# Performance work log

Measured on AMD Instinct MI355X. Metric: run time of the kernel, lower is better.

## Reference

```python
import jax, jax.numpy as jnp
import numpy as np

EPS_BN = 1e-4


def gcn_conv(x, W, b, src, dst):
    """PyG GCNConv with added self-loops and symmetric normalization."""
    N = x.shape[0]
    h = x @ W  # [N, out]
    # degree over targets, +1 for the implicit self-loop on every node
    deg = jnp.zeros((N,), x.dtype).at[dst].add(1.0) + 1.0
    dinv = jax.lax.rsqrt(deg)  # deg^{-1/2}
    norm = dinv[src] * dinv[dst]  # per-edge coefficient
    msg = h[src] * norm[:, None]  # [E, out] gather (memory-bound)
    out = jax.ops.segment_sum(msg, dst, num_segments=N)
    out = out + h * (dinv * dinv)[:, None]  # self-loop term, norm = 1/deg
    return out + b


def batch_norm(x, gamma, beta):
    # training-mode BN over the node dim, biased variance (matches torch train)
    m = jnp.mean(x, axis=0)
    v = jnp.mean(jnp.square(x - m), axis=0)
    return (x - m) * jax.lax.rsqrt(v + EPS_BN) * gamma + beta


def setup_inputs() -> dict:
    key = jax.random.key(0)
    ks = jax.random.split(key, 8)
    N, E, D = 100000, 1600000, 64
    L = 2
    x = jax.random.normal(ks[0], (N, D), jnp.float32)
    edge_index = jax.random.randint(ks[1], (2, E), 0, N, jnp.int32)
    batch = jnp.sort(jax.random.randint(ks[2], (N,), 0, 128, jnp.int32))
    s = 1.0 / np.sqrt(D)
    return {
        "x": x,
        "edge_index": edge_index,
        "batch": batch,
        "enc_W": jax.random.normal(ks[3], (L, D, D), jnp.float32) * s,
        "enc_b": jnp.zeros((L, D), jnp.float32),
        "enc_gamma": jnp.ones((L, D), jnp.float32),
        "enc_beta": jnp.zeros((L, D), jnp.float32),
        "attr_W": jax.random.normal(ks[4], (L, D, D), jnp.float32) * s,
        "attr_b": jnp.zeros((L, D), jnp.float32),
        "attr_gamma": jnp.ones((L, D), jnp.float32),
        "attr_beta": jnp.zeros((L, D), jnp.float32),
        "str_W": jax.random.normal(ks[5], (L, D, D), jnp.float32) * s,
        "str_b": jnp.zeros((L, D), jnp.float32),
        "str_gamma": jnp.ones((L, D), jnp.float32),
        "str_beta": jnp.zeros((L, D), jnp.float32),
    }


def reference(x, edge_index, batch, enc_W, enc_b, enc_gamma, enc_beta,
              attr_W, attr_b, attr_gamma, attr_beta,
              str_W, str_b, str_gamma, str_beta):
    src, dst = edge_index[0], edge_index[1]
    L = enc_W.shape[0]

    # ---- Encoder: GCN -> sigmoid -> (dropout id) -> BN ----
    h = x
    for i in range(L):
        h = gcn_conv(h, enc_W[i], enc_b[i], src, dst)
        h = jax.nn.sigmoid(h)
        h = batch_norm(h, enc_gamma[i], enc_beta[i])
    x_enc = h
    # x_pool = global_mean_pool(x_enc, batch) is computed but discarded upstream

    # ---- Attribute decoder: GCN -> (dropout) -> sigmoid (except last) -> BN ----
    h = x_enc
    for i in range(L):
        h = gcn_conv(h, attr_W[i], attr_b[i], src, dst)
        if i != L - 1:
            h = jax.nn.sigmoid(h)
        h = batch_norm(h, attr_gamma[i], attr_beta[i])
    x_att = h

    # ---- Structure decoder ----
    h = x_enc
    for i in range(L):
        h = gcn_conv(h, str_W[i], str_b[i], src, dst)
        if i != L - 1:
            h = jax.nn.sigmoid(h)
        else:
            h = jax.nn.sigmoid(h * 0.5)
        h = batch_norm(h, str_gamma[i], str_beta[i])
    x_str = h

    return (x_str, x_att, x_enc)
```

## Files before the change

### kernel.cpp

```cpp
#include <hip/hip_runtime.h>

#define D 64
#define BCH 4096

typedef __attribute__((ext_vector_type(8))) _Float16 f16x8;
typedef __attribute__((ext_vector_type(4))) float f32x4;

__device__ __forceinline__ float sigmoidf_(float x) {
    return 1.0f / (1.0f + __expf(-x));
}
__device__ __forceinline__ float h2f(ushort u) {
    _Float16 h;
    __builtin_memcpy(&h, &u, 2);
    return (float)h;
}
__device__ __forceinline__ ushort f2h(float f) {
    _Float16 h = (_Float16)f;
    ushort u;
    __builtin_memcpy(&u, &h, 2);
    return u;
}
__device__ __forceinline__ float2 up2(uint v) {
    float2 r;
    r.x = h2f((ushort)(v & 0xffffu));
    r.y = h2f((ushort)(v >> 16));
    return r;
}


__global__ __launch_bounds__(256) void bin_edges(const int* __restrict__ src,
                                                 const int* __restrict__ dst,
                                                 int* __restrict__ bcur,
                                                 int* __restrict__ binsrc,
                                                 int* __restrict__ bindst,
                                                 int CAP, int E) {
    __shared__ int lsrc[BCH], ldst[BCH];
    __shared__ int hist[128], base[128];
    int t = threadIdx.x;
    int e0 = blockIdx.x * BCH;
    if (t < 128) hist[t] = 0;
    __syncthreads();
    for (int k = t; k < BCH; k += 256) {
        int e = e0 + k;
        int d_ = -1, s_ = 0;
        if (e < E) {
            s_ = src[e];
            d_ = dst[e];
            atomicAdd(&hist[d_ >> 10], 1);
        }
        lsrc[k] = s_;
        ldst[k] = d_;
    }
    __syncthreads();
    if (t < 128) {
        int c = hist[t];
        base[t] = (c > 0) ? atomicAdd(&bcur[t], c) : 0;
        hist[t] = 0;
    }
    __syncthreads();
    for (int k = t; k < BCH; k += 256) {
        int d_ = ldst[k];
        if (d_ >= 0) {
            int b = d_ >> 10;
            int p = base[b] + atomicAdd(&hist[b], 1);
            binsrc[(size_t)b * CAP + p] = lsrc[k];
            bindst[(size_t)b * CAP + p] = d_;
        }
    }
}

__global__ __launch_bounds__(128) void scan_nb(const int* __restrict__ bcur,
                                               int* __restrict__ boff,
                                               int* __restrict__ csr,
                                               int NB, int N, int E) {
    __shared__ int tmp[128];
    int t = threadIdx.x;
    int v = (t < NB) ? bcur[t] : 0;
    tmp[t] = v;
    __syncthreads();
    for (int o = 1; o < 128; o <<= 1) {
        int x = (t >= o) ? tmp[t - o] : 0;
        __syncthreads();
        tmp[t] += x;
        __syncthreads();
    }
    if (t < NB) boff[t] = tmp[t] - v;
    if (t == 0) csr[N] = E;
}

__global__ __launch_bounds__(256) void build_csr(const int* __restrict__ binsrc,
                                                 const int* __restrict__ bindst,
                                                 const int* __restrict__ bcur,
                                                 const int* __restrict__ boff,
                                                 int* __restrict__ csr,
                                                 int* __restrict__ sorted,
                                                 float* __restrict__ dinv,
                                                 float* __restrict__ rdinv,
                                                 int CAP, int N) {
    __shared__ int hist[1024];
    __shared__ int part[256];
    int t = threadIdx.x;
    int b = blockIdx.x;
    int nb0 = b << 10;
    int cnt = bcur[b];
    int e0 = boff[b];
    const int* bs = binsrc + (size_t)b * CAP;
    const int* bd = bindst + (size_t)b * CAP;
    for (int k = t; k < 1024; k += 256) hist[k] = 0;
    __syncthreads();
    for (int k = t; k < cnt; k += 256) atomicAdd(&hist[bd[k] - nb0], 1);
    __syncthreads();
    int v0 = hist[4 * t], v1 = hist[4 * t + 1], v2 = hist[4 * t + 2], v3 = hist[4 * t + 3];
    part[t] = v0 + v1 + v2 + v3;
    __syncthreads();
    for (int o = 1; o < 256; o <<= 1) {
        int x = (t >= o) ? part[t - o] : 0;
        __syncthreads();
        part[t] += x;
        __syncthreads();
    }
    int run = (t > 0) ? part[t - 1] : 0;
    int pre[4];
    pre[0] = run;
    pre[1] = run + v0;
    pre[2] = run + v0 + v1;
    pre[3] = run + v0 + v1 + v2;
    int deg[4] = {v0, v1, v2, v3};
    __syncthreads();
    hist[4 * t + 0] = e0 + pre[0];
    hist[4 * t + 1] = e0 + pre[1];
    hist[4 * t + 2] = e0 + pre[2];
    hist[4 * t + 3] = e0 + pre[3];
#pragma unroll
    for (int j = 0; j < 4; j++) {
        int node = nb0 + 4 * t + j;
        if (node < N) {
            csr[node] = e0 + pre[j];
            float c = (float)deg[j] + 1.0f;
            dinv[node] = rsqrtf(c);
            rdinv[node] = sqrtf(c);
        }
    }
    __syncthreads();
    for (int k = t; k < cnt; k += 256) {
        int d_ = bd[k];
        int p = atomicAdd(&hist[d_ - nb0], 1);
        sorted[p] = bs[k];
    }
}


__global__ __launch_bounds__(256) void prep_xd(const float* __restrict__ x,
                                               const float* __restrict__ dinv,
                                               ushort* __restrict__ actd, int N16) {
    int p = blockIdx.x * 256 + threadIdx.x;
    if (p >= N16) return;
    int n = p >> 4;
    float d = dinv[n];
    float4 v = reinterpret_cast<const float4*>(x)[p];
    ushort4 o;
    o.x = f2h(v.x * d);
    o.y = f2h(v.y * d);
    o.z = f2h(v.z * d);
    o.w = f2h(v.w * d);
    reinterpret_cast<ushort4*>(actd)[p] = o;
}

__global__ __launch_bounds__(256) void wprep(const float* __restrict__ W,
                                             const float* __restrict__ Aaf,
                                             ushort* __restrict__ wfrag) {
    int idx = blockIdx.x * 256 + threadIdx.x;
    if (idx >= 4096) return;
    int i = idx & 7;
    int lane = (idx >> 3) & 63;
    int hc = idx >> 9;
    int h = hc >> 2, c = hc & 3;
    int k = h * 32 + (lane >> 4) * 8 + i;
    int j = c * 16 + (lane & 15);
    float w = W[k * 64 + j];
    if (Aaf) w *= Aaf[k];
    wfrag[idx] = f2h(w);
}


__global__ __launch_bounds__(256) void agg_g(const ushort* __restrict__ actd,
                                             const int* __restrict__ ptr,
                                             const int* __restrict__ srcs,
                                             const float* __restrict__ dinv,
                                             const float* __restrict__ rdinv,
                                             ushort* __restrict__ zh,
                                             float* __restrict__ ssum,
                                             float* __restrict__ sssq,
                                             float* __restrict__ qout, int N) {
    __shared__ float red[2][4][64];
    int lane = threadIdx.x & 63;
    int wv = threadIdx.x >> 6;
    int l = lane & 31, h = lane >> 5;
    const bool do_stats = (ssum != nullptr);
    const bool do_q = (qout != nullptr);
    float2 ps = make_float2(0.f, 0.f), pq = make_float2(0.f, 0.f);
    for (int n = blockIdx.x * 4 + wv; n < N; n += gridDim.x * 4) {
        int s = ptr[n], e = ptr[n + 1];
        uint selfu = *reinterpret_cast<const uint*>(actd + ((size_t)n << 6) + (l << 1));
        float2 sf = up2(selfu);
        float2 acc = (h == 0) ? sf : make_float2(0.f, 0.f);
        float dn = dinv[n];
        if (do_stats && h == 0) {
            float r = rdinv[n];
            float ax = sf.x * r, ay = sf.y * r;
            ps.x += ax; ps.y += ay;
            pq.x += ax * ax; pq.y += ay * ay;
        }
        float qa = 0.f;
        int i = s + h;
        for (; i + 6 < e; i += 8) {
            int u0 = srcs[i], u1 = srcs[i + 2], u2 = srcs[i + 4], u3 = srcs[i + 6];
            uint w0 = *reinterpret_cast<const uint*>(actd + ((size_t)u0 << 6) + (l << 1));
            uint w1 = *reinterpret_cast<const uint*>(actd + ((size_t)u1 << 6) + (l << 1));
            uint w2 = *reinterpret_cast<const uint*>(actd + ((size_t)u2 << 6) + (l << 1));
            uint w3 = *reinterpret_cast<const uint*>(actd + ((size_t)u3 << 6) + (l << 1));
            if (do_q && l == 0) qa += (dinv[u0] + dinv[u1]) + (dinv[u2] + dinv[u3]);
            float2 f0 = up2(w0), f1 = up2(w1), f2 = up2(w2), f3 = up2(w3);
            acc.x += (f0.x + f1.x) + (f2.x + f3.x);
            acc.y += (f0.y + f1.y) + (f2.y + f3.y);
        }
        for (; i < e; i += 2) {
            int u = srcs[i];
            uint w = *reinterpret_cast<const uint*>(actd + ((size_t)u << 6) + (l << 1));
            if (do_q && l == 0) qa += dinv[u];
            float2 f = up2(w);
            acc.x += f.x;
            acc.y += f.y;
        }
        acc.x += __shfl_xor(acc.x, 32);
        acc.y += __shfl_xor(acc.y, 32);
        if (do_q) {
            float qo = qa + __shfl(qa, 32);
            if (lane == 0) qout[n] = dn * (dn + qo);
        }
        if (h == 0) {
            uint pk = (uint)f2h(acc.x * dn) | ((uint)f2h(acc.y * dn) << 16);
            *reinterpret_cast<uint*>(zh + ((size_t)n << 6) + (l << 1)) = pk;
        }
    }
    if (do_stats) {
        if (h == 0) {
            red[0][wv][2 * l + 0] = ps.x;
            red[0][wv][2 * l + 1] = ps.y;
            red[1][wv][2 * l + 0] = pq.x;
            red[1][wv][2 * l + 1] = pq.y;
        }
        __syncthreads();
        if (wv == 0) {
            float t0 = red[0][0][lane] + red[0][1][lane] + red[0][2][lane] + red[0][3][lane];
            float t1 = red[1][0][lane] + red[1][1][lane] + red[1][2][lane] + red[1][3][lane];
            atomicAdd(&ssum[lane], t0);
            atomicAdd(&sssq[lane], t1);
        }
    }
}

__global__ __launch_bounds__(256) void agg_dual(const ushort* __restrict__ ab,
                                                const int* __restrict__ ptr,
                                                const int* __restrict__ srcs,
                                                const float* __restrict__ dinv,
                                                const float* __restrict__ rdinv,
                                                ushort* __restrict__ zab,
                                                float* __restrict__ ssA,
                                                float* __restrict__ sqA,
                                                float* __restrict__ ssS,
                                                float* __restrict__ sqS,
                                                int N, int E) {
    __shared__ float red[2][4][128];
    int lane = threadIdx.x & 63;
    int wv = threadIdx.x >> 6;
    int Em1 = E - 1;
    float2 ps = make_float2(0.f, 0.f), pq = make_float2(0.f, 0.f);
    for (int n = blockIdx.x * 4 + wv; n < N; n += gridDim.x * 4) {
        int s = ptr[n], e = ptr[n + 1];
        uint su = *reinterpret_cast<const uint*>(ab + ((size_t)n << 7) + (lane << 1));
        float2 acc = up2(su);
        {
            float r = rdinv[n];
            float ax = acc.x * r, ay = acc.y * r;
            ps.x += ax; ps.y += ay;
            pq.x += ax * ax; pq.y += ay * ay;
        }
        int i = s;
        for (; i + 7 < e; i += 8) {
            int u[8];
#pragma unroll
            for (int j = 0; j < 8; j++) u[j] = srcs[i + j];
#pragma unroll
            for (int j = 0; j < 8; j++) {
                uint v = *reinterpret_cast<const uint*>(ab + ((size_t)u[j] << 7) + (lane << 1));
                float2 f = up2(v);
                acc.x += f.x;
                acc.y += f.y;
            }
        }
        if (i < e) {
#pragma unroll
            for (int j = 0; j < 8; j++) {
                int idx = min(i + j, Em1);
                int u_ = srcs[idx];
                uint v = *reinterpret_cast<const uint*>(ab + ((size_t)u_ << 7) + (lane << 1));
                float w = (i + j < e) ? 1.0f : 0.0f;
                float2 f = up2(v);
                acc.x = fmaf(w, f.x, acc.x);
                acc.y = fmaf(w, f.y, acc.y);
            }
        }
        float dn = dinv[n];
        uint pk = (uint)f2h(acc.x * dn) | ((uint)f2h(acc.y * dn) << 16);
        *reinterpret_cast<uint*>(zab + ((size_t)n << 7) + (lane << 1)) = pk;
    }
    red[0][wv][2 * lane + 0] = ps.x;
    red[0][wv][2 * lane + 1] = ps.y;
    red[1][wv][2 * lane + 0] = pq.x;
    red[1][wv][2 * lane + 1] = pq.y;
    __syncthreads();
    if (wv == 0) {
#pragma unroll
        for (int m0 = 0; m0 < 2; m0++) {
            int m = lane + m0 * 64;
            float t0 = red[0][0][m] + red[0][1][m] + red[0][2][m] + red[0][3][m];
            float t1 = red[1][0][m] + red[1][1][m] + red[1][2][m] + red[1][3][m];
            if (m < 64) {
                atomicAdd(&ssA[m], t0);
                atomicAdd(&sqA[m], t1);
            } else {
                atomicAdd(&ssS[m - 64], t0);
                atomicAdd(&sqS[m - 64], t1);
            }
        }
    }
}


template <int MODE, bool HAS_AFF, bool OUT_HALF>
__global__ __launch_bounds__(256) void gemm_mfma(const ushort* __restrict__ zh, int is,
                                                 const ushort* __restrict__ wfrag,
                                                 const float* __restrict__ bias,
                                                 const float* __restrict__ u,
                                                 const float* __restrict__ q,
                                                 const float* __restrict__ dinv,
                                                 ushort* __restrict__ outh, int os,
                                                 float* __restrict__ outf,
                                                 float* __restrict__ ssum,
                                                 float* __restrict__ sssq, int N) {
    int tid = threadIdx.x;
    int lane = tid & 63;
    int wv = tid >> 6;
    int l15 = lane & 15;
    int lg = lane >> 4;
    int tb = blockIdx.x * 64;

    const ushort* zrow = zh + (size_t)(tb + wv * 16 + l15) * is + (lg << 3);
    f16x8 a0 = *reinterpret_cast<const f16x8*>(zrow);
    f16x8 a1 = *reinterpret_cast<const f16x8*>(zrow + 32);

    const f16x8* wf = reinterpret_cast<const f16x8*>(wfrag) + lane;

    f32x4 acc[4];
#pragma unroll
    for (int c = 0; c < 4; c++) {
        f32x4 t = {0.f, 0.f, 0.f, 0.f};
        t = __builtin_amdgcn_mfma_f32_16x16x32_f16(a0, wf[(0 * 4 + c) * 64], t, 0, 0, 0);
        t = __builtin_amdgcn_mfma_f32_16x16x32_f16(a1, wf[(1 * 4 + c) * 64], t, 0, 0, 0);
        acc[c] = t;
    }

    int rowbase = tb + wv * 16 + lg * 4;
    float qv[4], dv[4];
    bool vld[4];
#pragma unroll
    for (int r = 0; r < 4; r++) {
        int row = rowbase + r;
        vld[r] = row < N;
        qv[r] = (HAS_AFF && vld[r]) ? q[row] : 0.f;
        dv[r] = (OUT_HALF && vld[r]) ? dinv[row] : 0.f;
    }
    float sa[4], sq[4];
#pragma unroll
    for (int c = 0; c < 4; c++) { sa[c] = 0.f; sq[c] = 0.f; }

#pragma unroll
    for (int c = 0; c < 4; c++) {
        int col = c * 16 + l15;
        float bcol = bias[col];
        float ucol = HAS_AFF ? u[col] : 0.f;
#pragma unroll
        for (int r = 0; r < 4; r++) {
            if (!vld[r]) continue;
            float o = acc[c][r] + bcol;
            if (HAS_AFF) o = fmaf(qv[r], ucol, o);
            float a = (MODE == 0) ? sigmoidf_(o)
                                  : ((MODE == 1) ? o : sigmoidf_(0.5f * o));
            int row = rowbase + r;
            if (OUT_HALF) {
                outh[(size_t)row * os + col] = f2h(a * dv[r]);
            } else {
                outf[((size_t)row << 6) + col] = a;
                sa[c] += a;
                sq[c] += a * a;
            }
        }
    }

    if (!OUT_HALF) {
        __shared__ float red[2][4][4][16];
#pragma unroll
        for (int c = 0; c < 4; c++) {
            sa[c] += __shfl_xor(sa[c], 16);
            sa[c] += __shfl_xor(sa[c], 32);
            sq[c] += __shfl_xor(sq[c], 16);
            sq[c] += __shfl_xor(sq[c], 32);
        }
        if (lg == 0) {
#pragma unroll
            for (int c = 0; c < 4; c++) {
                red[0][wv][c][l15] = sa[c];
                red[1][wv][c][l15] = sq[c];
            }
        }
        __syncthreads();
        if (wv == 0) {
            int c = lane >> 4, l = lane & 15;
            float t0 = red[0][0][c][l] + red[0][1][c][l] + red[0][2][c][l] + red[0][3][c][l];
            float t1 = red[1][0][c][l] + red[1][1][c][l] + red[1][2][c][l] + red[1][3][c][l];
            atomicAdd(&ssum[lane], t0);
            atomicAdd(&sssq[lane], t1);
        }
    }
}


__global__ __launch_bounds__(64) void finalize_aff(const float* __restrict__ ssum,
                                                   const float* __restrict__ sssq,
                                                   const float* __restrict__ gamma,
                                                   const float* __restrict__ beta,
                                                   float* __restrict__ A,
                                                   float* __restrict__ C, float invN) {
    int c = threadIdx.x;
    float m = ssum[c] * invN;
    float var = sssq[c] * invN - m * m;
    float rs = rsqrtf(var + 1e-4f);
    float a = rs * gamma[c];
    A[c] = a;
    C[c] = fmaf(-m, a, beta[c]);
}

__global__ __launch_bounds__(64) void compute_u(const float* __restrict__ C,
                                                const float* __restrict__ W,
                                                float* __restrict__ u) {
    int j = threadIdx.x;
    float s = 0.f;
    for (int k = 0; k < 64; k++) s = fmaf(C[k], W[k * 64 + j], s);
    u[j] = s;
}

__global__ __launch_bounds__(256) void bn_apply_h(const ushort* __restrict__ actd,
                                                  const float* __restrict__ rdinv,
                                                  const float* __restrict__ A,
                                                  const float* __restrict__ C,
                                                  float* __restrict__ out, int N16) {
    int p = blockIdx.x * 256 + threadIdx.x;
    if (p >= N16) return;
    int n = p >> 4;
    int cb = (p & 15) * 4;
    float r = rdinv[n];
    ushort4 v = reinterpret_cast<const ushort4*>(actd)[p];
    float4 o;
    o.x = fmaf(h2f(v.x) * r, A[cb + 0], C[cb + 0]);
    o.y = fmaf(h2f(v.y) * r, A[cb + 1], C[cb + 1]);
    o.z = fmaf(h2f(v.z) * r, A[cb + 2], C[cb + 2]);
    o.w = fmaf(h2f(v.w) * r, A[cb + 3], C[cb + 3]);
    reinterpret_cast<float4*>(out)[p] = o;
}

__global__ __launch_bounds__(256) void bn_apply_f32(const float* __restrict__ act,
                                                    const float* __restrict__ A,
                                                    const float* __restrict__ C,
                                                    float* __restrict__ out, int N16) {
    int p = blockIdx.x * 256 + threadIdx.x;
    if (p >= N16) return;
    int cb = (p & 15) * 4;
    float4 v = reinterpret_cast<const float4*>(act)[p];
    float4 o;
    o.x = fmaf(v.x, A[cb + 0], C[cb + 0]);
    o.y = fmaf(v.y, A[cb + 1], C[cb + 1]);
    o.z = fmaf(v.z, A[cb + 2], C[cb + 2]);
    o.w = fmaf(v.w, A[cb + 3], C[cb + 3]);
    reinterpret_cast<float4*>(out)[p] = o;
}


extern "C" void kernel_launch(void* const* d_in, const int* in_sizes, int n_in,
                              void* d_out, int out_size, void* d_ws, size_t ws_size,
                              hipStream_t stream) {
    const int N = in_sizes[0] / D;
    const int E = in_sizes[1] / 2;

    const float* x = (const float*)d_in[0];
    const int* ei = (const int*)d_in[1];
    const int* src_in = ei;
    const int* dst_in = ei + E;
    const float* encW = (const float*)d_in[3];
    const float* encb = (const float*)d_in[4];
    const float* encg = (const float*)d_in[5];
    const float* encbe = (const float*)d_in[6];
    const float* attW = (const float*)d_in[7];
    const float* attb = (const float*)d_in[8];
    const float* attg = (const float*)d_in[9];
    const float* attbe = (const float*)d_in[10];
    const float* strW = (const float*)d_in[11];
    const float* strb = (const float*)d_in[12];
    const float* strg = (const float*)d_in[13];
    const float* strbe = (const float*)d_in[14];

    const int NB = (N + 1023) >> 10;
    int CAP = (E + NB - 1) / NB;
    CAP = CAP + CAP / 8 + 256;
    CAP = (CAP + 255) & ~255;

    char* ws = (char*)d_ws;
    size_t off = 0;
    auto alloc = [&](size_t bytes) -> char* {
        char* p = ws + off;
        off += (bytes + 255) & ~(size_t)255;
        return p;
    };
    int* csr = (int*)alloc((size_t)(N + 1) * 4);
    int* bcur = (int*)alloc(128 * 4);
    int* boff = (int*)alloc(128 * 4);
    float* dinv = (float*)alloc((size_t)N * 4);
    float* rdinv = (float*)alloc((size_t)N * 4);
    float* q = (float*)alloc((size_t)N * 4);
    float* stats = (float*)alloc(6 * 128 * 4);
    float* aff = (float*)alloc(6 * 128 * 4);
    float* ubuf = (float*)alloc(6 * 64 * 4);
    ushort* wf = (ushort*)alloc(6 * 4096 * 2);
    int* sorted = (int*)alloc((size_t)E * 4);
    ushort* zh = (ushort*)alloc((size_t)(N + 64) * 64 * 2);
    size_t binbytes = 2 * (size_t)NB * CAP * 4;
    size_t zabbytes = (size_t)(N + 64) * 128 * 2;
    char* region = alloc(binbytes > zabbytes ? binbytes : zabbytes);
    int* binsrc = (int*)region;
    int* bindst = binsrc + (size_t)NB * CAP;
    ushort* zab = (ushort*)region;
    float* fbuf = (float*)alloc((size_t)N * 64 * 4);
    ushort* hB = (ushort*)fbuf;
    ushort* hA = hB + (size_t)N * 64;
    ushort* hAB = (ushort*)alloc((size_t)(N + 64) * 128 * 2);

    float* out_str = (float*)d_out;
    float* out_att = out_str + (size_t)N * D;
    float* out_enc = out_att + (size_t)N * D;

    hipMemsetAsync(bcur, 0, 128 * 4, stream);
    hipMemsetAsync(stats, 0, 6 * 128 * 4, stream);

    int N16 = N * 16;
    int g16 = (N16 + 255) / 256;
    int gT = (N + 63) / 64;
    float invN = 1.0f / (float)N;

    float* A0 = aff + 0 * 128; float* C0 = A0 + 64;
    float* A1 = aff + 1 * 128; float* C1 = A1 + 64;
    float* A2 = aff + 2 * 128; float* C2 = A2 + 64;
    float* A3 = aff + 3 * 128; float* C3 = A3 + 64;
    float* A4 = aff + 4 * 128; float* C4 = A4 + 64;
    float* A5 = aff + 5 * 128; float* C5 = A5 + 64;
    ushort* wf0 = wf + 0 * 4096;
    ushort* wf1 = wf + 1 * 4096;
    ushort* wf2 = wf + 2 * 4096;
    ushort* wf3 = wf + 3 * 4096;
    ushort* wf4 = wf + 4 * 4096;
    ushort* wf5 = wf + 5 * 4096;

    bin_edges<<<(E + BCH - 1) / BCH, 256, 0, stream>>>(src_in, dst_in, bcur,
                                                       binsrc, bindst, CAP, E);
    scan_nb<<<1, 128, 0, stream>>>(bcur, boff, csr, NB, N, E);
    build_csr<<<NB, 256, 0, stream>>>(binsrc, bindst, bcur, boff, csr, sorted,
                                      dinv, rdinv, CAP, N);

    prep_xd<<<g16, 256, 0, stream>>>(x, dinv, hA, N16);
    wprep<<<16, 256, 0, stream>>>(encW, nullptr, wf0);
    agg_g<<<2048, 256, 0, stream>>>(hA, csr, sorted, dinv, rdinv, zh,
                                    nullptr, nullptr, q, N);
    gemm_mfma<0, false, true><<<gT, 256, 0, stream>>>(zh, 64, wf0, encb, nullptr,
                                                      q, dinv, hB, 64, nullptr,
                                                      nullptr, nullptr, N);
    agg_g<<<2048, 256, 0, stream>>>(hB, csr, sorted, dinv, rdinv, zh,
                                    stats + 0, stats + 64, nullptr, N);
    finalize_aff<<<1, 64, 0, stream>>>(stats + 0, stats + 64, encg, encbe, A0, C0, invN);
    compute_u<<<1, 64, 0, stream>>>(C0, encW + 4096, ubuf + 0);
    wprep<<<16, 256, 0, stream>>>(encW + 4096, A0, wf1);
    gemm_mfma<0, true, true><<<gT, 256, 0, stream>>>(zh, 64, wf1, encb + 64, ubuf + 0,
                                                     q, dinv, hA, 64, nullptr,
                                                     nullptr, nullptr, N);
    agg_g<<<2048, 256, 0, stream>>>(hA, csr, sorted, dinv, rdinv, zh,
                                    stats + 128, stats + 192, nullptr, N);
    finalize_aff<<<1, 64, 0, stream>>>(stats + 128, stats + 192, encg + 64,
                                       encbe + 64, A1, C1, invN);
    compute_u<<<1, 64, 0, stream>>>(C1, attW, ubuf + 64);
    compute_u<<<1, 64, 0, stream>>>(C1, strW, ubuf + 128);
    wprep<<<16, 256, 0, stream>>>(attW, A1, wf2);
    wprep<<<16, 256, 0, stream>>>(strW, A1, wf3);
    bn_apply_h<<<g16, 256, 0, stream>>>(hA, rdinv, A1, C1, out_enc, N16);
    gemm_mfma<0, true, true><<<gT, 256, 0, stream>>>(zh, 64, wf2, attb, ubuf + 64,
                                                     q, dinv, hAB, 128, nullptr,
                                                     nullptr, nullptr, N);
    gemm_mfma<0, true, true><<<gT, 256, 0, stream>>>(zh, 64, wf3, strb, ubuf + 128,
                                                     q, dinv, hAB + 64, 128, nullptr,
                                                     nullptr, nullptr, N);
    agg_dual<<<2048, 256, 0, stream>>>(hAB, csr, sorted, dinv, rdinv, zab,
                                       stats + 256, stats + 320,
                                       stats + 512, stats + 576, N, E);
    finalize_aff<<<1, 64, 0, stream>>>(stats + 256, stats + 320, attg, attbe,
                                       A2, C2, invN);
    compute_u<<<1, 64, 0, stream>>>(C2, attW + 4096, ubuf + 192);
    wprep<<<16, 256, 0, stream>>>(attW + 4096, A2, wf4);
    gemm_mfma<1, true, false><<<gT, 256, 0, stream>>>(zab, 128, wf4, attb + 64,
                                                      ubuf + 192, q, dinv,
                                                      nullptr, 0, fbuf,
                                                      stats + 384, stats + 448, N);
    finalize_aff<<<1, 64, 0, stream>>>(stats + 384, stats + 448, attg + 64,
                                       attbe + 64, A3, C3, invN);
    bn_apply_f32<<<g16, 256, 0, stream>>>(fbuf, A3, C3, out_att, N16);
    finalize_aff<<<1, 64, 0, stream>>>(stats + 512, stats + 576, strg, strbe,
                                       A4, C4, invN);
    compute_u<<<1, 64, 0, stream>>>(C4, strW + 4096, ubuf + 320);
    wprep<<<16, 256, 0, stream>>>(strW + 4096, A4, wf5);
    gemm_mfma<2, true, false><<<gT, 256, 0, stream>>>(zab + 64, 128, wf5, strb + 64,
                                                      ubuf + 320, q, dinv,
                                                      nullptr, 0, fbuf,
                                                      stats + 640, stats + 704, N);
    finalize_aff<<<1, 64, 0, stream>>>(stats + 640, stats + 704, strg + 64,
                                       strbe + 64, A5, C5, invN);
    bn_apply_f32<<<g16, 256, 0, stream>>>(fbuf, A5, C5, out_str, N16);
}
```

Before: 651.4 us.

## Fuse BN prep kernels, merge decoder GEMMs, recompute final GEMMs instead of f32 roundtrip

Merges finalize_aff, compute_u and wprep into a single layer_prep kernel per layer, cutting small-kernel launches. The two first-layer decoder GEMMs become one gemm_dual kernel that reads zh once. The final GEMMs now run twice: once to gather BN statistics and once to write the normalized output directly, replacing the f32 intermediate buffer and the bn_apply_f32 pass. agg_g and agg_dual load source indices eight at a time with readlane and prefetch the next batch, and agg_g switches to one 16-bit element per lane across all 64 lanes instead of two-halves-per-edge processing.

```diff
diff --git a/kernel.cpp b/kernel.cpp
--- a/kernel.cpp
+++ b/kernel.cpp
@@ -167,7 +167,6 @@
 }
 
 __global__ __launch_bounds__(256) void wprep(const float* __restrict__ W,
-                                             const float* __restrict__ Aaf,
                                              ushort* __restrict__ wfrag) {
     int idx = blockIdx.x * 256 + threadIdx.x;
     if (idx >= 4096) return;
@@ -177,9 +176,62 @@
     int h = hc >> 2, c = hc & 3;
     int k = h * 32 + (lane >> 4) * 8 + i;
     int j = c * 16 + (lane & 15);
-    float w = W[k * 64 + j];
-    if (Aaf) w *= Aaf[k];
-    wfrag[idx] = f2h(w);
+    wfrag[idx] = f2h(W[k * 64 + j]);
+}
+
+__global__ __launch_bounds__(256) void layer_prep(const float* __restrict__ ssum,
+                                                  const float* __restrict__ sssq,
+                                                  const float* __restrict__ gamma,
+                                                  const float* __restrict__ beta,
+                                                  const float* __restrict__ W,
+                                                  float* __restrict__ A,
+                                                  float* __restrict__ C,
+                                                  float* __restrict__ u,
+                                                  ushort* __restrict__ wfrag,
+                                                  float invN) {
+    __shared__ float As[64], Cs[64];
+    int t = threadIdx.x;
+    if (t < 64) {
+        float m = ssum[t] * invN;
+        float var = sssq[t] * invN - m * m;
+        float rs = rsqrtf(var + 1e-4f);
+        float a = rs * gamma[t];
+        As[t] = a;
+        A[t] = a;
+        float c = fmaf(-m, a, beta[t]);
+        Cs[t] = c;
+        C[t] = c;
+    }
+    __syncthreads();
+    if (t < 64) {
+        float s = 0.f;
+        for (int k = 0; k < 64; k++) s = fmaf(Cs[k], W[k * 64 + t], s);
+        u[t] = s;
+    }
+    for (int idx = t; idx < 4096; idx += 256) {
+        int i = idx & 7;
+        int lane = (idx >> 3) & 63;
+        int hc = idx >> 9;
+        int h = hc >> 2, c = hc & 3;
+        int k = h * 32 + (lane >> 4) * 8 + i;
+        int j = c * 16 + (lane & 15);
+        wfrag[idx] = f2h(W[k * 64 + j] * As[k]);
+    }
+}
+
+__global__ __launch_bounds__(64) void finalize_aff(const float* __restrict__ ssum,
+                                                   const float* __restrict__ sssq,
+                                                   const float* __restrict__ gamma,
+                                                   const float* __restrict__ beta,
+                                                   float* __restrict__ A,
+                                                   float* __restrict__ C, float invN) {
+    int c = threadIdx.x;
+    float m = ssum[c] * invN;
+    float var = sssq[c] * invN - m * m;
+    float rs = rsqrtf(var + 1e-4f);
+    float a = rs * gamma[c];
+    A[c] = a;
+    C[c] = fmaf(-m, a, beta[c]);
 }
 
 
@@ -191,65 +243,56 @@
                                              ushort* __restrict__ zh,
                                              float* __restrict__ ssum,
                                              float* __restrict__ sssq,
-                                             float* __restrict__ qout, int N) {
+                                             float* __restrict__ qout, int N, int E) {
     __shared__ float red[2][4][64];
     int lane = threadIdx.x & 63;
     int wv = threadIdx.x >> 6;
-    int l = lane & 31, h = lane >> 5;
+    int Em1 = E - 1;
     const bool do_stats = (ssum != nullptr);
     const bool do_q = (qout != nullptr);
-    float2 ps = make_float2(0.f, 0.f), pq = make_float2(0.f, 0.f);
+    float ps = 0.f, pq = 0.f;
     for (int n = blockIdx.x * 4 + wv; n < N; n += gridDim.x * 4) {
         int s = ptr[n], e = ptr[n + 1];
-        uint selfu = *reinterpret_cast<const uint*>(actd + ((size_t)n << 6) + (l << 1));
-        float2 sf = up2(selfu);
-        float2 acc = (h == 0) ? sf : make_float2(0.f, 0.f);
+        float self = h2f(actd[((size_t)n << 6) + lane]);
+        float acc = self;
         float dn = dinv[n];
-        if (do_stats && h == 0) {
-            float r = rdinv[n];
-            float ax = sf.x * r, ay = sf.y * r;
-            ps.x += ax; ps.y += ay;
-            pq.x += ax * ax; pq.y += ay * ay;
+        if (do_stats) {
+            float a = self * rdinv[n];
+            ps += a;
+            pq += a * a;
         }
         float qa = 0.f;
-        int i = s + h;
-        for (; i + 6 < e; i += 8) {
-            int u0 = srcs[i], u1 = srcs[i + 2], u2 = srcs[i + 4], u3 = srcs[i + 6];
-            uint w0 = *reinterpret_cast<const uint*>(actd + ((size_t)u0 << 6) + (l << 1));
-            uint w1 = *reinterpret_cast<const uint*>(actd + ((size_t)u1 << 6) + (l << 1));
-            uint w2 = *reinterpret_cast<const uint*>(actd + ((size_t)u2 << 6) + (l << 1));
-            uint w3 = *reinterpret_cast<const uint*>(actd + ((size_t)u3 << 6) + (l << 1));
-            if (do_q && l == 0) qa += (dinv[u0] + dinv[u1]) + (dinv[u2] + dinv[u3]);
-            float2 f0 = up2(w0), f1 = up2(w1), f2 = up2(w2), f3 = up2(w3);
-            acc.x += (f0.x + f1.x) + (f2.x + f3.x);
-            acc.y += (f0.y + f1.y) + (f2.y + f3.y);
-        }
-        for (; i < e; i += 2) {
-            int u = srcs[i];
-            uint w = *reinterpret_cast<const uint*>(actd + ((size_t)u << 6) + (l << 1));
-            if (do_q && l == 0) qa += dinv[u];
-            float2 f = up2(w);
-            acc.x += f.x;
-            acc.y += f.y;
-        }
-        acc.x += __shfl_xor(acc.x, 32);
-        acc.y += __shfl_xor(acc.y, 32);
-        if (do_q) {
-            float qo = qa + __shfl(qa, 32);
-            if (lane == 0) qout[n] = dn * (dn + qo);
-        }
-        if (h == 0) {
-            uint pk = (uint)f2h(acc.x * dn) | ((uint)f2h(acc.y * dn) << 16);
-            *reinterpret_cast<uint*>(zh + ((size_t)n << 6) + (l << 1)) = pk;
-        }
+        int i = s;
+        int idx8 = srcs[min(i + (lane & 7), Em1)];
+        while (i + 8 <= e) {
+            int ni = i + 8;
+            int nidx = srcs[min(ni + (lane & 7), Em1)];
+#pragma unroll
+            for (int j = 0; j < 8; j++) {
+                int u = __builtin_amdgcn_readlane(idx8, j);
+                float f = h2f(actd[((size_t)u << 6) + lane]);
+                acc += f;
+                if (do_q) qa += dinv[u];
+            }
+            idx8 = nidx;
+            i = ni;
+        }
+        if (i < e) {
+#pragma unroll
+            for (int j = 0; j < 8; j++) {
+                int u = __builtin_amdgcn_readlane(idx8, j);
+                float f = h2f(actd[((size_t)u << 6) + lane]);
+                float w = (i + j < e) ? 1.0f : 0.0f;
+                acc = fmaf(w, f, acc);
+                if (do_q) qa = fmaf(w, dinv[u], qa);
+            }
+        }
+        if (do_q && lane == 0) qout[n] = dn * (dn + qa);
+        zh[((size_t)n << 6) + lane] = f2h(acc * dn);
     }
     if (do_stats) {
-        if (h == 0) {
-            red[0][wv][2 * l + 0] = ps.x;
-            red[0][wv][2 * l + 1] = ps.y;
-            red[1][wv][2 * l + 0] = pq.x;
-            red[1][wv][2 * l + 1] = pq.y;
-        }
+        red[0][wv][lane] = ps;
+        red[1][wv][lane] = pq;
         __syncthreads();
         if (wv == 0) {
             float t0 = red[0][0][lane] + red[0][1][lane] + red[0][2][lane] + red[0][3][lane];
@@ -287,24 +330,26 @@
             pq.x += ax * ax; pq.y += ay * ay;
         }
         int i = s;
-        for (; i + 7 < e; i += 8) {
-            int u[8];
-#pragma unroll
-            for (int j = 0; j < 8; j++) u[j] = srcs[i + j];
+        int idx8 = srcs[min(i + (lane & 7), Em1)];
+        while (i + 8 <= e) {
+            int ni = i + 8;
+            int nidx = srcs[min(ni + (lane & 7), Em1)];
 #pragma unroll
             for (int j = 0; j < 8; j++) {
-                uint v = *reinterpret_cast<const uint*>(ab + ((size_t)u[j] << 7) + (lane << 1));
+                int u = __builtin_amdgcn_readlane(idx8, j);
+                uint v = *reinterpret_cast<const uint*>(ab + ((size_t)u << 7) + (lane << 1));
                 float2 f = up2(v);
                 acc.x += f.x;
                 acc.y += f.y;
             }
+            idx8 = nidx;
+            i = ni;
         }
         if (i < e) {
 #pragma unroll
             for (int j = 0; j < 8; j++) {
-                int idx = min(i + j, Em1);
-                int u_ = srcs[idx];
-                uint v = *reinterpret_cast<const uint*>(ab + ((size_t)u_ << 7) + (lane << 1));
+                int u = __builtin_amdgcn_readlane(idx8, j);
+                uint v = *reinterpret_cast<const uint*>(ab + ((size_t)u << 7) + (lane << 1));
                 float w = (i + j < e) ? 1.0f : 0.0f;
                 float2 f = up2(v);
                 acc.x = fmaf(w, f.x, acc.x);
@@ -337,8 +382,7 @@
     }
 }
 
-
-template <int MODE, bool HAS_AFF, bool OUT_HALF>
+template <int MODE, bool HAS_AFF, int OM>
 __global__ __launch_bounds__(256) void gemm_mfma(const ushort* __restrict__ zh, int is,
                                                  const ushort* __restrict__ wfrag,
                                                  const float* __restrict__ bias,
@@ -347,8 +391,8 @@
                                                  const float* __restrict__ dinv,
                                                  ushort* __restrict__ outh, int os,
                                                  float* __restrict__ outf,
-                                                 float* __restrict__ ssum,
-                                                 float* __restrict__ sssq, int N) {
+                                                 float* __restrict__ s0,
+                                                 float* __restrict__ s1, int N) {
     int tid = threadIdx.x;
     int lane = tid & 63;
     int wv = tid >> 6;
@@ -379,7 +423,7 @@
         int row = rowbase + r;
         vld[r] = row < N;
         qv[r] = (HAS_AFF && vld[r]) ? q[row] : 0.f;
-        dv[r] = (OUT_HALF && vld[r]) ? dinv[row] : 0.f;
+        dv[r] = (OM == 0 && vld[r]) ? dinv[row] : 0.f;
     }
     float sa[4], sq[4];
 #pragma unroll
@@ -390,6 +434,8 @@
         int col = c * 16 + l15;
         float bcol = bias[col];
         float ucol = HAS_AFF ? u[col] : 0.f;
+        float Acol = (OM == 2) ? s0[col] : 0.f;
+        float Ccol = (OM == 2) ? s1[col] : 0.f;
 #pragma unroll
         for (int r = 0; r < 4; r++) {
             if (!vld[r]) continue;
@@ -398,17 +444,18 @@
             float a = (MODE == 0) ? sigmoidf_(o)
                                   : ((MODE == 1) ? o : sigmoidf_(0.5f * o));
             int row = rowbase + r;
-            if (OUT_HALF) {
+            if (OM == 0) {
                 outh[(size_t)row * os + col] = f2h(a * dv[r]);
-            } else {
-                outf[((size_t)row << 6) + col] = a;
+            } else if (OM == 1) {
                 sa[c] += a;
                 sq[c] += a * a;
+            } else {
+                outf[((size_t)row << 6) + col] = fmaf(a, Acol, Ccol);
             }
         }
     }
 
-    if (!OUT_HALF) {
+    if (OM == 1) {
         __shared__ float red[2][4][4][16];
 #pragma unroll
         for (int c = 0; c < 4; c++) {
@@ -429,35 +476,76 @@
             int c = lane >> 4, l = lane & 15;
             float t0 = red[0][0][c][l] + red[0][1][c][l] + red[0][2][c][l] + red[0][3][c][l];
             float t1 = red[1][0][c][l] + red[1][1][c][l] + red[1][2][c][l] + red[1][3][c][l];
-            atomicAdd(&ssum[lane], t0);
-            atomicAdd(&sssq[lane], t1);
-        }
-    }
-}
-
-
-__global__ __launch_bounds__(64) void finalize_aff(const float* __restrict__ ssum,
-                                                   const float* __restrict__ sssq,
-                                                   const float* __restrict__ gamma,
-                                                   const float* __restrict__ beta,
-                                                   float* __restrict__ A,
-                                                   float* __restrict__ C, float invN) {
-    int c = threadIdx.x;
-    float m = ssum[c] * invN;
-    float var = sssq[c] * invN - m * m;
-    float rs = rsqrtf(var + 1e-4f);
-    float a = rs * gamma[c];
-    A[c] = a;
-    C[c] = fmaf(-m, a, beta[c]);
-}
-
-__global__ __launch_bounds__(64) void compute_u(const float* __restrict__ C,
-                                                const float* __restrict__ W,
-                                                float* __restrict__ u) {
-    int j = threadIdx.x;
-    float s = 0.f;
-    for (int k = 0; k < 64; k++) s = fmaf(C[k], W[k * 64 + j], s);
-    u[j] = s;
+            atomicAdd(&s0[lane], t0);
+            atomicAdd(&s1[lane], t1);
+        }
+    }
+}
+
+__global__ __launch_bounds__(256) void gemm_dual(const ushort* __restrict__ zh,
+                                                 const ushort* __restrict__ wfA,
+                                                 const ushort* __restrict__ wfS,
+                                                 const float* __restrict__ bA,
+                                                 const float* __restrict__ bS,
+                                                 const float* __restrict__ uA,
+                                                 const float* __restrict__ uS,
+                                                 const float* __restrict__ q,
+                                                 const float* __restrict__ dinv,
+                                                 ushort* __restrict__ outAB, int N) {
+    int tid = threadIdx.x;
+    int lane = tid & 63;
+    int wv = tid >> 6;
+    int l15 = lane & 15;
+    int lg = lane >> 4;
+    int tb = blockIdx.x * 64;
+
+    const ushort* zrow = zh + ((size_t)(tb + wv * 16 + l15) << 6) + (lg << 3);
+    f16x8 a0 = *reinterpret_cast<const f16x8*>(zrow);
+    f16x8 a1 = *reinterpret_cast<const f16x8*>(zrow + 32);
+
+    const f16x8* wa = reinterpret_cast<const f16x8*>(wfA) + lane;
+    const f16x8* wsp = reinterpret_cast<const f16x8*>(wfS) + lane;
+
+    f32x4 accA[4], accS[4];
+#pragma unroll
+    for (int c = 0; c < 4; c++) {
+        f32x4 t = {0.f, 0.f, 0.f, 0.f};
+        t = __builtin_amdgcn_mfma_f32_16x16x32_f16(a0, wa[(0 * 4 + c) * 64], t, 0, 0, 0);
+        t = __builtin_amdgcn_mfma_f32_16x16x32_f16(a1, wa[(1 * 4 + c) * 64], t, 0, 0, 0);
+        accA[c] = t;
+        f32x4 t2 = {0.f, 0.f, 0.f, 0.f};
+        t2 = __builtin_amdgcn_mfma_f32_16x16x32_f16(a0, wsp[(0 * 4 + c) * 64], t2, 0, 0, 0);
+        t2 = __builtin_amdgcn_mfma_f32_16x16x32_f16(a1, wsp[(1 * 4 + c) * 64], t2, 0, 0, 0);
+        accS[c] = t2;
+    }
+
+    int rowbase = tb + wv * 16 + lg * 4;
+    float qv[4], dv[4];
+    bool vld[4];
+#pragma unroll
+    for (int r = 0; r < 4; r++) {
+        int row = rowbase + r;
+        vld[r] = row < N;
+        qv[r] = vld[r] ? q[row] : 0.f;
+        dv[r] = vld[r] ? dinv[row] : 0.f;
+    }
+#pragma unroll
+    for (int c = 0; c < 4; c++) {
+        int col = c * 16 + l15;
+        float bcA = bA[col], ucA = uA[col];
+        float bcS = bS[col], ucS = uS[col];
+#pragma unroll
+        for (int r = 0; r < 4; r++) {
+            if (!vld[r]) continue;
+            int row = rowbase + r;
+            float oA = fmaf(qv[r], ucA, accA[c][r] + bcA);
+            float oS = fmaf(qv[r], ucS, accS[c][r] + bcS);
+            float aA = sigmoidf_(oA);
+            float aS = sigmoidf_(oS);
+            outAB[((size_t)row << 7) + col] = f2h(aA * dv[r]);
+            outAB[((size_t)row << 7) + 64 + col] = f2h(aS * dv[r]);
+        }
+    }
 }
 
 __global__ __launch_bounds__(256) void bn_apply_h(const ushort* __restrict__ actd,
@@ -476,22 +564,6 @@
     o.y = fmaf(h2f(v.y) * r, A[cb + 1], C[cb + 1]);
     o.z = fmaf(h2f(v.z) * r, A[cb + 2], C[cb + 2]);
     o.w = fmaf(h2f(v.w) * r, A[cb + 3], C[cb + 3]);
-    reinterpret_cast<float4*>(out)[p] = o;
-}
-
-__global__ __launch_bounds__(256) void bn_apply_f32(const float* __restrict__ act,
-                                                    const float* __restrict__ A,
-                                                    const float* __restrict__ C,
-                                                    float* __restrict__ out, int N16) {
-    int p = blockIdx.x * 256 + threadIdx.x;
-    if (p >= N16) return;
-    int cb = (p & 15) * 4;
-    float4 v = reinterpret_cast<const float4*>(act)[p];
-    float4 o;
-    o.x = fmaf(v.x, A[cb + 0], C[cb + 0]);
-    o.y = fmaf(v.y, A[cb + 1], C[cb + 1]);
-    o.z = fmaf(v.z, A[cb + 2], C[cb + 2]);
-    o.w = fmaf(v.w, A[cb + 3], C[cb + 3]);
     reinterpret_cast<float4*>(out)[p] = o;
 }
 
@@ -549,9 +621,8 @@
     int* binsrc = (int*)region;
     int* bindst = binsrc + (size_t)NB * CAP;
     ushort* zab = (ushort*)region;
-    float* fbuf = (float*)alloc((size_t)N * 64 * 4);
-    ushort* hB = (ushort*)fbuf;
-    ushort* hA = hB + (size_t)N * 64;
+    ushort* hA = (ushort*)alloc((size_t)N * 64 * 2);
+    ushort* hB = (ushort*)alloc((size_t)N * 64 * 2);
     ushort* hAB = (ushort*)alloc((size_t)(N + 64) * 128 * 2);
 
     float* out_str = (float*)d_out;
@@ -586,58 +657,49 @@
                                       dinv, rdinv, CAP, N);
 
     prep_xd<<<g16, 256, 0, stream>>>(x, dinv, hA, N16);
-    wprep<<<16, 256, 0, stream>>>(encW, nullptr, wf0);
+    wprep<<<16, 256, 0, stream>>>(encW, wf0);
     agg_g<<<2048, 256, 0, stream>>>(hA, csr, sorted, dinv, rdinv, zh,
-                                    nullptr, nullptr, q, N);
-    gemm_mfma<0, false, true><<<gT, 256, 0, stream>>>(zh, 64, wf0, encb, nullptr,
-                                                      q, dinv, hB, 64, nullptr,
-                                                      nullptr, nullptr, N);
+                                    nullptr, nullptr, q, N, E);
+    gemm_mfma<0, false, 0><<<gT, 256, 0, stream>>>(zh, 64, wf0, encb, nullptr,
+                                                   q, dinv, hB, 64, nullptr,
+                                                   nullptr, nullptr, N);
     agg_g<<<2048, 256, 0, stream>>>(hB, csr, sorted, dinv, rdinv, zh,
-                                    stats + 0, stats + 64, nullptr, N);
-    finalize_aff<<<1, 64, 0, stream>>>(stats + 0, stats + 64, encg, encbe, A0, C0, invN);
-    compute_u<<<1, 64, 0, stream>>>(C0, encW + 4096, ubuf + 0);
-    wprep<<<16, 256, 0, stream>>>(encW + 4096, A0, wf1);
-    gemm_mfma<0, true, true><<<gT, 256, 0, stream>>>(zh, 64, wf1, encb + 64, ubuf + 0,
-                                                     q, dinv, hA, 64, nullptr,
-                                                     nullptr, nullptr, N);
+                                    stats + 0, stats + 64, nullptr, N, E);
+    layer_prep<<<1, 256, 0, stream>>>(stats + 0, stats + 64, encg, encbe,
+                                      encW + 4096, A0, C0, ubuf + 0, wf1, invN);
+    gemm_mfma<0, true, 0><<<gT, 256, 0, stream>>>(zh, 64, wf1, encb + 64, ubuf + 0,
+                                                  q, dinv, hA, 64, nullptr,
+                                                  nullptr, nullptr, N);
     agg_g<<<2048, 256, 0, stream>>>(hA, csr, sorted, dinv, rdinv, zh,
-                                    stats + 128, stats + 192, nullptr, N);
-    finalize_aff<<<1, 64, 0, stream>>>(stats + 128, stats + 192, encg + 64,
-                                       encbe + 64, A1, C1, invN);
-    compute_u<<<1, 64, 0, stream>>>(C1, attW, ubuf + 64);
-    compute_u<<<1, 64, 0, stream>>>(C1, strW, ubuf + 128);
-    wprep<<<16, 256, 0, stream>>>(attW, A1, wf2);
-    wprep<<<16, 256, 0, stream>>>(strW, A1, wf3);
+                                    stats + 128, stats + 192, nullptr, N, E);
+    layer_prep<<<1, 256, 0, stream>>>(stats + 128, stats + 192, encg + 64,
+                                      encbe + 64, attW, A1, C1, ubuf + 64, wf2, invN);
+    layer_prep<<<1, 256, 0, stream>>>(stats + 128, stats + 192, encg + 64,
+                                      encbe + 64, strW, A1, C1, ubuf + 128, wf3, invN);
     bn_apply_h<<<g16, 256, 0, stream>>>(hA, rdinv, A1, C1, out_enc, N16);
-    gemm_mfma<0, true, true><<<gT, 256, 0, stream>>>(zh, 64, wf2, attb, ubuf + 64,
-                                                     q, dinv, hAB, 128, nullptr,
-                                                     nullptr, nullptr, N);
-    gemm_mfma<0, true, true><<<gT, 256, 0, stream>>>(zh, 64, wf3, strb, ubuf + 128,
-                                                     q, dinv, hAB + 64, 128, nullptr,
-                                                     nullptr, nullptr, N);
+    gemm_dual<<<gT, 256, 0, stream>>>(zh, wf2, wf3, attb, strb, ubuf + 64,
+                                      ubuf + 128, q, dinv, hAB, N);
     agg_dual<<<2048, 256, 0, stream>>>(hAB, csr, sorted, dinv, rdinv, zab,
                                        stats + 256, stats + 320,
                                        stats + 512, stats + 576, N, E);
-    finalize_aff<<<1, 64, 0, stream>>>(stats + 256, stats + 320, attg, attbe,
-                                       A2, C2, invN);
-    compute_u<<<1, 64, 0, stream>>>(C2, attW + 4096, ubuf + 192);
-    wprep<<<16, 256, 0, stream>>>(attW + 4096, A2, wf4);
-    gemm_mfma<1, true, false><<<gT, 256, 0, stream>>>(zab, 128, wf4, attb + 64,
-                                                      ubuf + 192, q, dinv,
-                                                      nullptr, 0, fbuf,
-                                                      stats + 384, stats + 448, N);
+    layer_prep<<<1, 256, 0, stream>>>(stats + 256, stats + 320, attg, attbe,
+                                      attW + 4096, A2, C2, ubuf + 192, wf4, invN);
+    gemm_mfma<1, true, 1><<<gT, 256, 0, stream>>>(zab, 128, wf4, attb + 64,
+                                                  ubuf + 192, q, dinv, nullptr, 0,
+                                                  nullptr, stats + 384, stats + 448, N);
     finalize_aff<<<1, 64, 0, stream>>>(stats + 384, stats + 448, attg + 64,
                                        attbe + 64, A3, C3, invN);
-    bn_apply_f32<<<g16, 256, 0, stream>>>(fbuf, A3, C3, out_att, N16);
-    finalize_aff<<<1, 64, 0, stream>>>(stats + 512, stats + 576, strg, strbe,
-                                       A4, C4, invN);
-    compute_u<<<1, 64, 0, stream>>>(C4, strW + 4096, ubuf + 320);
-    wprep<<<16, 256, 0, stream>>>(strW + 4096, A4, wf5);
-    gemm_mfma<2, true, false><<<gT, 256, 0, stream>>>(zab + 64, 128, wf5, strb + 64,
-                                                      ubuf + 320, q, dinv,
-                                                      nullptr, 0, fbuf,
-                                                      stats + 640, stats + 704, N);
+    gemm_mfma<1, true, 2><<<gT, 256, 0, stream>>>(zab, 128, wf4, attb + 64,
+                                                  ubuf + 192, q, dinv, nullptr, 0,
+                                                  out_att, A3, C3, N);
+    layer_prep<<<1, 256, 0, stream>>>(stats + 512, stats + 576, strg, strbe,
+                                      strW + 4096, A4, C4, ubuf + 320, wf5, invN);
+    gemm_mfma<2, true, 1><<<gT, 256, 0, stream>>>(zab + 64, 128, wf5, strb + 64,
+                                                  ubuf + 320, q, dinv, nullptr, 0,
+                                                  nullptr, stats + 640, stats + 704, N);
     finalize_aff<<<1, 64, 0, stream>>>(stats + 640, stats + 704, strg + 64,
                                        strbe + 64, A5, C5, invN);
-    bn_apply_f32<<<g16, 256, 0, stream>>>(fbuf, A5, C5, out_str, N16);
-}
+    gemm_mfma<2, true, 2><<<gT, 256, 0, stream>>>(zab + 64, 128, wf5, strb + 64,
+                                                  ubuf + 320, q, dinv, nullptr, 0,
+                                                  out_str, A5, C5, N);
+}
```

Result: faster. 604.9 us (-7.1%).
